# Optimization experiments

Measured on AMD Instinct MI355X. Metric: run time of the kernel, lower is better.

## Reference

```python
import jax, jax.numpy as jnp
import numpy as np

B, D, C, T = 2048, 512, 128, 151  # batch, hidden, vocab(NUM_CHAR), TEXT_MAX_LEN


def setup_inputs() -> dict:
    key = jax.random.key(0)
    ks = jax.random.split(key, 8)
    s = 1.0 / np.sqrt(D)
    u = lambda k, shape: jax.random.uniform(k, shape, jnp.float32, -s, s)
    return {
        "feat": jax.random.normal(ks[0], (B, D), jnp.float32),  # resnet pooler_output
        "W_ih": u(ks[1], (3 * D, D)),   # GRU input weights (r,z,n stacked, torch layout)
        "W_hh": u(ks[2], (3 * D, D)),   # GRU hidden weights
        "b_ih": u(ks[3], (3 * D,)),
        "b_hh": u(ks[4], (3 * D,)),
        "W_proj": u(ks[5], (C, D)),     # Linear(512, NUM_CHAR)
        "b_proj": u(ks[6], (C,)),
        "embed": jax.random.normal(ks[7], (C, D), jnp.float32),  # Embedding(NUM_CHAR, 512)
    }


def reference(feat, W_ih, W_hh, b_ih, b_hh, W_proj, b_proj, embed):
    def step(carry, _):
        h, x = carry  # [B,D] each
        gi = x @ W_ih.T + b_ih   # [B,3D]
        gh = h @ W_hh.T + b_hh   # [B,3D]
        i_r, i_z, i_n = jnp.split(gi, 3, axis=1)
        h_r, h_z, h_n = jnp.split(gh, 3, axis=1)
        r = jax.nn.sigmoid(i_r + h_r)
        z = jax.nn.sigmoid(i_z + h_z)
        n = jnp.tanh(i_n + r * h_n)
        h_new = (1.0 - z) * n + z * h
        logits = h_new @ W_proj.T + b_proj          # [B,C]
        probs = jax.nn.softmax(logits, axis=1)
        tok = jnp.argmax(probs, axis=1)             # [B]
        x_new = embed[tok]                          # greedy feedback
        return (h_new, x_new), (logits, tok)

    h0 = feat                                        # hidden init = pooled feature
    x0 = jnp.zeros((feat.shape[0], D), feat.dtype)   # zero start token input
    _, (logits_seq, toks_seq) = jax.lax.scan(step, (h0, x0), None, length=T)
    logits = jnp.transpose(logits_seq, (1, 2, 0))    # [B, NUM_CHAR, T]
    tokens = toks_seq.T                              # [B, T]
    return logits, tokens
```

## Files before the change

kernel.cpp:

```cpp
#include <hip/hip_runtime.h>
#include <math.h>

#define BB 2048
#define DD 512
#define CC 128
#define TT 151
#define G3 1536

typedef __bf16 bf16x8 __attribute__((ext_vector_type(8)));
typedef float f32x4 __attribute__((ext_vector_type(4)));


__global__ void k_transpose_wih(const float* __restrict__ Wih, float* __restrict__ WihT) {
    int idx = blockIdx.x * 256 + threadIdx.x;
    if (idx < G3 * DD) {
        int j = idx / DD, k = idx - j * DD;
        WihT[k * G3 + j] = Wih[idx];
    }
}

__global__ void k_pack_wp(const float* __restrict__ Wproj, float4* __restrict__ Wp4) {
    int idx = blockIdx.x * 256 + threadIdx.x;
    if (idx >= CC * 128) return;
    int c = idx >> 7, k4 = idx & 127;
    float4 v = *(const float4*)&Wproj[c * DD + k4 * 4];
    Wp4[k4 * CC + c] = v;
}

__global__ void k_pack_whh_frag(const float* __restrict__ Whh, __bf16* __restrict__ out) {
    int idx = blockIdx.x * 256 + threadIdx.x;
    if (idx >= 786432) return;
    int j8 = idx & 7;
    int lane = (idx >> 3) & 63;
    int rest = idx >> 9;
    int tile = rest % 12;
    int kt = (rest / 12) % 16;
    int w = rest / (12 * 16);
    int g = tile >> 2, tl = tile & 3;
    int col = lane & 15, quad = lane >> 4;
    int jcol = g * 512 + w * 64 + tl * 16 + col;
    int k = kt * 32 + quad * 8 + j8;
    float v = Whh[jcol * DD + k];
    __bf16 hi = (__bf16)v;
    __bf16 lo = (__bf16)(v - (float)hi);
    size_t base = ((((size_t)w * 16 + kt) * 12 + tile) * 2) * 512 + lane * 8 + j8;
    out[base] = hi;
    out[base + 512] = lo;
}

__global__ void k_build_E(const float* __restrict__ embed, const float* __restrict__ WihT,
                          const float* __restrict__ b_ih, const float* __restrict__ b_hh,
                          float* __restrict__ E) {
    __shared__ float emb[16][DD];
    const int t = threadIdx.x;
    const int j = blockIdx.x * 256 + t;
    const int c0 = blockIdx.y * 16;
    for (int i = 0; i < 16; i++) {
        int c = c0 + i;
        for (int k = t; k < DD; k += 256)
            emb[i][k] = (c < CC) ? embed[c * DD + k] : 0.0f;
    }
    __syncthreads();
    float acc[16];
#pragma unroll
    for (int i = 0; i < 16; i++) acc[i] = 0.0f;
    for (int k = 0; k < DD; k++) {
        float w = WihT[k * G3 + j];
#pragma unroll
        for (int i = 0; i < 16; i++) acc[i] = fmaf(emb[i][k], w, acc[i]);
    }
    float bj = b_ih[j] + (j < 1024 ? b_hh[j] : 0.0f);
    for (int i = 0; i < 16; i++) {
        int c = c0 + i;
        if (c <= CC) E[(size_t)c * G3 + j] = acc[i] + bj;
    }
}


__device__ __forceinline__ float fast_sigmoid(float x) {
    return __builtin_amdgcn_rcpf(1.0f + __expf(-x));
}
__device__ __forceinline__ float fast_tanh(float x) {
    x = fminf(10.0f, fmaxf(-10.0f, x));
    float e = __expf(2.0f * x);
    return (e - 1.0f) * __builtin_amdgcn_rcpf(e + 1.0f);
}

__global__ __launch_bounds__(512, 2) void k_gru(
    const float* __restrict__ feat, const __bf16* __restrict__ Whf,
    const float4* __restrict__ Wp4, const float* __restrict__ b_proj,
    const float* __restrict__ b_hh, const float* __restrict__ Ep,
    float* __restrict__ out) {
    __shared__ __align__(16) float h[8][DD];
    __shared__ __align__(16) __bf16 h_hi[16][520];
    __shared__ __align__(16) __bf16 h_lo[16][520];
    __shared__ float plg[4][8][CC];
    __shared__ float lgbuf[8][CC][9];
    __shared__ int tok_s[8];

    float* out_logits = out;
    float* out_tok = out + (size_t)BB * CC * TT;

    const int t = threadIdx.x;
    const int w = t >> 6;
    const int lane = t & 63;
    const int row0 = blockIdx.x * 8;

    for (int i = t; i < 16 * 520; i += 512) {
        ((__bf16*)h_hi)[i] = (__bf16)0.0f;
        ((__bf16*)h_lo)[i] = (__bf16)0.0f;
    }
    __syncthreads();
    for (int b = 0; b < 8; b++) {
        float v = feat[(size_t)(row0 + b) * DD + t];
        h[b][t] = v;
        __bf16 hi = (__bf16)v;
        h_hi[b][t] = hi;
        h_lo[b][t] = (__bf16)(v - (float)hi);
    }
    if (t < 8) tok_s[t] = CC;
    __syncthreads();

    const float bp0 = b_proj[lane];
    const float bp1 = b_proj[lane + 64];
    float bhn_t[4];
#pragma unroll
    for (int tile = 0; tile < 4; tile++)
        bhn_t[tile] = b_hh[1024 + w * 64 + tile * 16 + (lane & 15)];

    const __bf16* wseq = Whf + (size_t)w * 196608;
    const int am = lane & 15, aq = lane >> 4;

    for (int step = 0; step < TT; step++) {
        f32x4 acc[12];
#pragma unroll
        for (int i = 0; i < 12; i++) acc[i] = (f32x4)(0.0f);
        for (int kt = 0; kt < 16; kt++) {
            bf16x8 ahi = *(const bf16x8*)&h_hi[am][kt * 32 + aq * 8];
            bf16x8 alo = *(const bf16x8*)&h_lo[am][kt * 32 + aq * 8];
            const __bf16* wk = wseq + kt * 12288;
#pragma unroll
            for (int tile = 0; tile < 12; tile++) {
                bf16x8 bhi = *(const bf16x8*)(wk + tile * 1024 + lane * 8);
                bf16x8 blo = *(const bf16x8*)(wk + tile * 1024 + 512 + lane * 8);
                acc[tile] = __builtin_amdgcn_mfma_f32_16x16x32_bf16(ahi, bhi, acc[tile], 0, 0, 0);
                acc[tile] = __builtin_amdgcn_mfma_f32_16x16x32_bf16(alo, bhi, acc[tile], 0, 0, 0);
                acc[tile] = __builtin_amdgcn_mfma_f32_16x16x32_bf16(ahi, blo, acc[tile], 0, 0, 0);
            }
        }
        __syncthreads();

        if (lane < 32) {
            const int dcol = lane & 15;
            const int bq = (lane >> 4) * 4;
#pragma unroll
            for (int tile = 0; tile < 4; tile++) {
                const int d = w * 64 + tile * 16 + dcol;
#pragma unroll
                for (int rg = 0; rg < 4; rg++) {
                    const int b = bq + rg;
                    const float* Er = Ep + (size_t)tok_s[b] * G3 + d;
                    float rr = fast_sigmoid(acc[tile][rg] + Er[0]);
                    float zz = fast_sigmoid(acc[4 + tile][rg] + Er[512]);
                    float nn = fast_tanh(Er[1024] + rr * (acc[8 + tile][rg] + bhn_t[tile]));
                    float ho = h[b][d];
                    float hv = (1.0f - zz) * nn + zz * ho;
                    h[b][d] = hv;
                    __bf16 hi = (__bf16)hv;
                    h_hi[b][d] = hi;
                    h_lo[b][d] = (__bf16)(hv - (float)hi);
                }
            }
        }
        __syncthreads();

        {
            const int c = t & (CC - 1);
            const int q = t >> 7;
            float s[8];
#pragma unroll
            for (int b = 0; b < 8; b++) s[b] = 0.f;
            const int kb4 = q * 32;
#pragma unroll 4
            for (int k4 = 0; k4 < 32; k4++) {
                float4 wv = Wp4[(kb4 + k4) * CC + c];
#pragma unroll
                for (int b = 0; b < 8; b++) {
                    float4 hv = *(const float4*)&h[b][(kb4 + k4) * 4];
                    s[b] = fmaf(hv.x, wv.x, fmaf(hv.y, wv.y, fmaf(hv.z, wv.z, fmaf(hv.w, wv.w, s[b]))));
                }
            }
#pragma unroll
            for (int b = 0; b < 8; b++) plg[q][b][c] = s[b];
        }
        __syncthreads();

        {
            const int b = w;
            float v0 = plg[0][b][lane] + plg[1][b][lane] + plg[2][b][lane] + plg[3][b][lane] + bp0;
            float v1 = plg[0][b][lane + 64] + plg[1][b][lane + 64] + plg[2][b][lane + 64] +
                       plg[3][b][lane + 64] + bp1;
            const int sl = step & 7;
            lgbuf[b][lane][sl] = v0;
            lgbuf[b][lane + 64][sl] = v1;
            float bv; int bi;
            if (v0 >= v1) { bv = v0; bi = lane; } else { bv = v1; bi = lane + 64; }
#pragma unroll
            for (int off = 32; off > 0; off >>= 1) {
                float ov = __shfl_down(bv, off, 64);
                int oi = __shfl_down(bi, off, 64);
                if (ov > bv || (ov == bv && oi < bi)) { bv = ov; bi = oi; }
            }
            if (lane == 0) {
                tok_s[b] = bi;
                __builtin_nontemporal_store((float)bi, &out_tok[(size_t)(row0 + b) * TT + step]);
            }
        }
        __syncthreads();

        if ((step & 7) == 7 || step == TT - 1) {
            const int t0 = step & ~7;
            const int cnt = step - t0 + 1;
#pragma unroll
            for (int p = 0; p < 2; p++) {
                const int pair = t + p * 512;
                const int b = pair >> 7, c = pair & (CC - 1);
                float* dst = out_logits + ((size_t)(row0 + b) * CC + c) * TT + t0;
                const float* src = &lgbuf[b][c][0];
                for (int s = 0; s < cnt; s++) __builtin_nontemporal_store(src[s], &dst[s]);
            }
        }
    }
}


extern "C" void kernel_launch(void* const* d_in, const int* in_sizes, int n_in,
                              void* d_out, int out_size, void* d_ws, size_t ws_size,
                              hipStream_t stream) {
    const float* feat   = (const float*)d_in[0];
    const float* W_ih   = (const float*)d_in[1];
    const float* W_hh   = (const float*)d_in[2];
    const float* b_ih   = (const float*)d_in[3];
    const float* b_hh   = (const float*)d_in[4];
    const float* W_proj = (const float*)d_in[5];
    const float* b_proj = (const float*)d_in[6];
    const float* embed  = (const float*)d_in[7];
    float* out = (float*)d_out;

    float* ws = (float*)d_ws;
    float*  WihT = ws;
    float*  E    = ws + 786432;
    float4* Wp4  = (float4*)(ws + 984576);
    __bf16* Whf  = (__bf16*)(ws + 1050112);

    hipLaunchKernelGGL(k_transpose_wih, dim3(3072), dim3(256), 0, stream, W_ih, WihT);
    hipLaunchKernelGGL(k_pack_wp, dim3(64), dim3(256), 0, stream, W_proj, Wp4);
    hipLaunchKernelGGL(k_pack_whh_frag, dim3(3072), dim3(256), 0, stream, W_hh, Whf);
    hipLaunchKernelGGL(k_build_E, dim3(6, 9), dim3(256), 0, stream, embed, WihT, b_ih, b_hh, E);
    hipLaunchKernelGGL(k_gru, dim3(256), dim3(512), 0, stream,
                       feat, Whf, Wp4, b_proj, b_hh, E, out);
}
```

Before: 6.394 ms.

## Process 16 rows per block and compute projection with split-bf16 MFMA

Each block now handles 16 batch rows instead of 8, so the MFMA M dimension of 16 is fully used and every weight fragment read serves twice as many rows. The grid halves to 128 blocks. The fp32 projection loop is replaced by a 3-pass hi/lo bf16 MFMA against a newly packed W_proj fragment layout, and the hidden state now lives in registers instead of fp32 shared memory. This removes the plg partial-sum buffer and one reduction stage. The cost is fewer blocks than the 256 CUs, so each step's latency chain runs on half the grid, plus a larger lgbuf in shared memory.

```diff
diff --git a/kernel.cpp b/kernel.cpp
--- a/kernel.cpp
+++ b/kernel.cpp
@@ -19,12 +19,19 @@
     }
 }
 
-__global__ void k_pack_wp(const float* __restrict__ Wproj, float4* __restrict__ Wp4) {
+__global__ void k_pack_wp_frag(const float* __restrict__ Wproj, __bf16* __restrict__ out) {
     int idx = blockIdx.x * 256 + threadIdx.x;
-    if (idx >= CC * 128) return;
-    int c = idx >> 7, k4 = idx & 127;
-    float4 v = *(const float4*)&Wproj[c * DD + k4 * 4];
-    Wp4[k4 * CC + c] = v;
+    if (idx >= 131072) return;
+    int j = idx & 7;
+    int lane = (idx >> 3) & 63;
+    int part = (idx >> 9) & 1;
+    int kt = (idx >> 10) & 15;
+    int w = idx >> 14;
+    int c = w * 16 + (lane & 15);
+    int k = kt * 32 + (lane >> 4) * 8 + j;
+    float v = Wproj[c * DD + k];
+    __bf16 hi = (__bf16)v;
+    out[idx] = part ? (__bf16)(v - (float)hi) : hi;
 }
 
 __global__ void k_pack_whh_frag(const float* __restrict__ Whh, __bf16* __restrict__ out) {
@@ -37,8 +44,8 @@
     int kt = (rest / 12) % 16;
     int w = rest / (12 * 16);
     int g = tile >> 2, tl = tile & 3;
-    int col = lane & 15, quad = lane >> 4;
-    int jcol = g * 512 + w * 64 + tl * 16 + col;
+    int colc = lane & 15, quad = lane >> 4;
+    int jcol = g * 512 + w * 64 + tl * 16 + colc;
     int k = kt * 32 + quad * 8 + j8;
     float v = Whh[jcol * DD + k];
     __bf16 hi = (__bf16)v;
@@ -65,9 +72,9 @@
 #pragma unroll
     for (int i = 0; i < 16; i++) acc[i] = 0.0f;
     for (int k = 0; k < DD; k++) {
-        float w = WihT[k * G3 + j];
-#pragma unroll
-        for (int i = 0; i < 16; i++) acc[i] = fmaf(emb[i][k], w, acc[i]);
+        float wv = WihT[k * G3 + j];
+#pragma unroll
+        for (int i = 0; i < 16; i++) acc[i] = fmaf(emb[i][k], wv, acc[i]);
     }
     float bj = b_ih[j] + (j < 1024 ? b_hh[j] : 0.0f);
     for (int i = 0; i < 16; i++) {
@@ -88,15 +95,13 @@
 
 __global__ __launch_bounds__(512, 2) void k_gru(
     const float* __restrict__ feat, const __bf16* __restrict__ Whf,
-    const float4* __restrict__ Wp4, const float* __restrict__ b_proj,
+    const __bf16* __restrict__ Wpf, const float* __restrict__ b_proj,
     const float* __restrict__ b_hh, const float* __restrict__ Ep,
     float* __restrict__ out) {
-    __shared__ __align__(16) float h[8][DD];
     __shared__ __align__(16) __bf16 h_hi[16][520];
     __shared__ __align__(16) __bf16 h_lo[16][520];
-    __shared__ float plg[4][8][CC];
-    __shared__ float lgbuf[8][CC][9];
-    __shared__ int tok_s[8];
+    __shared__ float lgbuf[16][CC][9];
+    __shared__ int tok_s[16];
 
     float* out_logits = out;
     float* out_tok = out + (size_t)BB * CC * TT;
@@ -104,40 +109,46 @@
     const int t = threadIdx.x;
     const int w = t >> 6;
     const int lane = t & 63;
-    const int row0 = blockIdx.x * 8;
-
-    for (int i = t; i < 16 * 520; i += 512) {
-        ((__bf16*)h_hi)[i] = (__bf16)0.0f;
-        ((__bf16*)h_lo)[i] = (__bf16)0.0f;
-    }
+    const int row0 = blockIdx.x * 16;
+    const int col = lane & 15;
+    const int quad = lane >> 4;
+    const int bq = quad * 4;
+
+    float ho[4][4];
+#pragma unroll
+    for (int tile = 0; tile < 4; tile++) {
+        const int d = w * 64 + tile * 16 + col;
+#pragma unroll
+        for (int rg = 0; rg < 4; rg++) {
+            const int b = bq + rg;
+            float v = feat[(size_t)(row0 + b) * DD + d];
+            ho[tile][rg] = v;
+            __bf16 hi = (__bf16)v;
+            h_hi[b][d] = hi;
+            h_lo[b][d] = (__bf16)(v - (float)hi);
+        }
+    }
+    if (t < 16) tok_s[t] = CC;
+
+    const float bp = b_proj[w * 16 + col];
+    float bhn_t[4];
+#pragma unroll
+    for (int tile = 0; tile < 4; tile++)
+        bhn_t[tile] = b_hh[1024 + w * 64 + tile * 16 + col];
+
+    const __bf16* wseq = Whf + (size_t)w * 196608;
+    const __bf16* wpseq = Wpf + (size_t)w * 16384;
     __syncthreads();
-    for (int b = 0; b < 8; b++) {
-        float v = feat[(size_t)(row0 + b) * DD + t];
-        h[b][t] = v;
-        __bf16 hi = (__bf16)v;
-        h_hi[b][t] = hi;
-        h_lo[b][t] = (__bf16)(v - (float)hi);
-    }
-    if (t < 8) tok_s[t] = CC;
-    __syncthreads();
-
-    const float bp0 = b_proj[lane];
-    const float bp1 = b_proj[lane + 64];
-    float bhn_t[4];
-#pragma unroll
-    for (int tile = 0; tile < 4; tile++)
-        bhn_t[tile] = b_hh[1024 + w * 64 + tile * 16 + (lane & 15)];
-
-    const __bf16* wseq = Whf + (size_t)w * 196608;
-    const int am = lane & 15, aq = lane >> 4;
 
     for (int step = 0; step < TT; step++) {
+        const int sl = step & 7;
+
         f32x4 acc[12];
 #pragma unroll
         for (int i = 0; i < 12; i++) acc[i] = (f32x4)(0.0f);
         for (int kt = 0; kt < 16; kt++) {
-            bf16x8 ahi = *(const bf16x8*)&h_hi[am][kt * 32 + aq * 8];
-            bf16x8 alo = *(const bf16x8*)&h_lo[am][kt * 32 + aq * 8];
+            bf16x8 ahi = *(const bf16x8*)&h_hi[col][kt * 32 + quad * 8];
+            bf16x8 alo = *(const bf16x8*)&h_lo[col][kt * 32 + quad * 8];
             const __bf16* wk = wseq + kt * 12288;
 #pragma unroll
             for (int tile = 0; tile < 12; tile++) {
@@ -150,22 +161,22 @@
         }
         __syncthreads();
 
-        if (lane < 32) {
-            const int dcol = lane & 15;
-            const int bq = (lane >> 4) * 4;
+        {
+            int tk[4];
+#pragma unroll
+            for (int rg = 0; rg < 4; rg++) tk[rg] = tok_s[bq + rg];
 #pragma unroll
             for (int tile = 0; tile < 4; tile++) {
-                const int d = w * 64 + tile * 16 + dcol;
+                const int d = w * 64 + tile * 16 + col;
 #pragma unroll
                 for (int rg = 0; rg < 4; rg++) {
                     const int b = bq + rg;
-                    const float* Er = Ep + (size_t)tok_s[b] * G3 + d;
+                    const float* Er = Ep + (size_t)tk[rg] * G3 + d;
                     float rr = fast_sigmoid(acc[tile][rg] + Er[0]);
                     float zz = fast_sigmoid(acc[4 + tile][rg] + Er[512]);
                     float nn = fast_tanh(Er[1024] + rr * (acc[8 + tile][rg] + bhn_t[tile]));
-                    float ho = h[b][d];
-                    float hv = (1.0f - zz) * nn + zz * ho;
-                    h[b][d] = hv;
+                    float hv = (1.0f - zz) * nn + zz * ho[tile][rg];
+                    ho[tile][rg] = hv;
                     __bf16 hi = (__bf16)hv;
                     h_hi[b][d] = hi;
                     h_lo[b][d] = (__bf16)(hv - (float)hi);
@@ -175,45 +186,41 @@
         __syncthreads();
 
         {
-            const int c = t & (CC - 1);
-            const int q = t >> 7;
-            float s[8];
-#pragma unroll
-            for (int b = 0; b < 8; b++) s[b] = 0.f;
-            const int kb4 = q * 32;
-#pragma unroll 4
-            for (int k4 = 0; k4 < 32; k4++) {
-                float4 wv = Wp4[(kb4 + k4) * CC + c];
-#pragma unroll
-                for (int b = 0; b < 8; b++) {
-                    float4 hv = *(const float4*)&h[b][(kb4 + k4) * 4];
-                    s[b] = fmaf(hv.x, wv.x, fmaf(hv.y, wv.y, fmaf(hv.z, wv.z, fmaf(hv.w, wv.w, s[b]))));
+            f32x4 accp = (f32x4)(0.0f);
+            for (int kt = 0; kt < 16; kt++) {
+                bf16x8 ahi = *(const bf16x8*)&h_hi[col][kt * 32 + quad * 8];
+                bf16x8 alo = *(const bf16x8*)&h_lo[col][kt * 32 + quad * 8];
+                const __bf16* pk = wpseq + kt * 1024;
+                bf16x8 bhi = *(const bf16x8*)(pk + lane * 8);
+                bf16x8 blo = *(const bf16x8*)(pk + 512 + lane * 8);
+                accp = __builtin_amdgcn_mfma_f32_16x16x32_bf16(ahi, bhi, accp, 0, 0, 0);
+                accp = __builtin_amdgcn_mfma_f32_16x16x32_bf16(alo, bhi, accp, 0, 0, 0);
+                accp = __builtin_amdgcn_mfma_f32_16x16x32_bf16(ahi, blo, accp, 0, 0, 0);
+            }
+#pragma unroll
+            for (int rg = 0; rg < 4; rg++)
+                lgbuf[bq + rg][w * 16 + col][sl] = accp[rg] + bp;
+        }
+        __syncthreads();
+
+        {
+#pragma unroll
+            for (int pass = 0; pass < 2; pass++) {
+                const int r = w * 2 + pass;
+                float v0 = lgbuf[r][lane][sl];
+                float v1 = lgbuf[r][lane + 64][sl];
+                float bv; int bi;
+                if (v0 >= v1) { bv = v0; bi = lane; } else { bv = v1; bi = lane + 64; }
+#pragma unroll
+                for (int off = 32; off > 0; off >>= 1) {
+                    float ov = __shfl_down(bv, off, 64);
+                    int oi = __shfl_down(bi, off, 64);
+                    if (ov > bv || (ov == bv && oi < bi)) { bv = ov; bi = oi; }
                 }
-            }
-#pragma unroll
-            for (int b = 0; b < 8; b++) plg[q][b][c] = s[b];
-        }
-        __syncthreads();
-
-        {
-            const int b = w;
-            float v0 = plg[0][b][lane] + plg[1][b][lane] + plg[2][b][lane] + plg[3][b][lane] + bp0;
-            float v1 = plg[0][b][lane + 64] + plg[1][b][lane + 64] + plg[2][b][lane + 64] +
-                       plg[3][b][lane + 64] + bp1;
-            const int sl = step & 7;
-            lgbuf[b][lane][sl] = v0;
-            lgbuf[b][lane + 64][sl] = v1;
-            float bv; int bi;
-            if (v0 >= v1) { bv = v0; bi = lane; } else { bv = v1; bi = lane + 64; }
-#pragma unroll
-            for (int off = 32; off > 0; off >>= 1) {
-                float ov = __shfl_down(bv, off, 64);
-                int oi = __shfl_down(bi, off, 64);
-                if (ov > bv || (ov == bv && oi < bi)) { bv = ov; bi = oi; }
-            }
-            if (lane == 0) {
-                tok_s[b] = bi;
-                __builtin_nontemporal_store((float)bi, &out_tok[(size_t)(row0 + b) * TT + step]);
+                if (lane == 0) {
+                    tok_s[r] = bi;
+                    __builtin_nontemporal_store((float)bi, &out_tok[(size_t)(row0 + r) * TT + step]);
+                }
             }
         }
         __syncthreads();
@@ -222,7 +229,7 @@
             const int t0 = step & ~7;
             const int cnt = step - t0 + 1;
 #pragma unroll
-            for (int p = 0; p < 2; p++) {
+            for (int p = 0; p < 4; p++) {
                 const int pair = t + p * 512;
                 const int b = pair >> 7, c = pair & (CC - 1);
                 float* dst = out_logits + ((size_t)(row0 + b) * CC + c) * TT + t0;
@@ -250,13 +257,13 @@
     float* ws = (float*)d_ws;
     float*  WihT = ws;
     float*  E    = ws + 786432;
-    float4* Wp4  = (float4*)(ws + 984576);
+    __bf16* Wpf  = (__bf16*)(ws + 984576);
     __bf16* Whf  = (__bf16*)(ws + 1050112);
 
     hipLaunchKernelGGL(k_transpose_wih, dim3(3072), dim3(256), 0, stream, W_ih, WihT);
-    hipLaunchKernelGGL(k_pack_wp, dim3(64), dim3(256), 0, stream, W_proj, Wp4);
+    hipLaunchKernelGGL(k_pack_wp_frag, dim3(512), dim3(256), 0, stream, W_proj, Wpf);
     hipLaunchKernelGGL(k_pack_whh_frag, dim3(3072), dim3(256), 0, stream, W_hh, Whf);
     hipLaunchKernelGGL(k_build_E, dim3(6, 9), dim3(256), 0, stream, embed, WihT, b_ih, b_hh, E);
-    hipLaunchKernelGGL(k_gru, dim3(256), dim3(512), 0, stream,
-                       feat, Whf, Wp4, b_proj, b_hh, E, out);
-}
+    hipLaunchKernelGGL(k_gru, dim3(128), dim3(512), 0, stream,
+                       feat, Whf, Wpf, b_proj, b_hh, E, out);
+}
```

Result: faster. 5.868 ms (-8.2%).
